# Optimization experiments

Measured on AMD Instinct MI355X. Metric: run time of the kernel, lower is better.

## Reference

```python
import jax, jax.numpy as jnp
import numpy as np

ALPHA = 0.8
TOPK = 9
LOW_BOUND = 0.0
EPS = 1e-10
IOU_EPS = 1e-6


def pairwise_iou(boxes1, boxes2):
    # boxes1 [N,4], boxes2 [G,4] in x1,y1,x2,y2 -> IoU [N,G] (mmdet BboxOverlaps2D)
    area1 = (boxes1[:, 2] - boxes1[:, 0]) * (boxes1[:, 3] - boxes1[:, 1])  # [N]
    area2 = (boxes2[:, 2] - boxes2[:, 0]) * (boxes2[:, 3] - boxes2[:, 1])  # [G]
    lt = jnp.maximum(boxes1[:, None, :2], boxes2[None, :, :2])  # [N,G,2]
    rb = jnp.minimum(boxes1[:, None, 2:], boxes2[None, :, 2:])  # [N,G,2]
    wh = jnp.clip(rb - lt, 0.0)
    inter = wh[..., 0] * wh[..., 1]  # [N,G]
    union = area1[:, None] + area2[None, :] - inter
    return inter / jnp.maximum(union, IOU_EPS)


def setup_inputs() -> dict:
    key = jax.random.key(0)
    k1, k2, k3, k4, k5, k6, k7 = jax.random.split(key, 7)
    N, G, C = 65536, 256, 80
    IMG = 1024.0
    points = jax.random.uniform(k1, (N, 2), dtype=jnp.float32) * IMG  # (cy, cx)
    p_xy1 = jax.random.uniform(k2, (N, 2), dtype=jnp.float32) * (IMG - 96.0)
    p_wh = jax.random.uniform(k3, (N, 2), dtype=jnp.float32) * 95.0 + 1.0
    bbox_preds = jnp.concatenate([p_xy1, p_xy1 + p_wh], axis=1)  # valid x1y1x2y2
    g_xy1 = jax.random.uniform(k4, (G, 2), dtype=jnp.float32) * (IMG - 256.0)
    g_wh = jax.random.uniform(k5, (G, 2), dtype=jnp.float32) * 255.0 + 1.0
    gt_bboxes = jnp.concatenate([g_xy1, g_xy1 + g_wh], axis=1)
    cls_scores = jax.random.normal(k6, (N, C), dtype=jnp.float32)
    gt_labels = jax.random.randint(k7, (G,), 0, C)
    return {"points": points, "cls_scores": cls_scores, "bbox_preds": bbox_preds,
            "gt_bboxes": gt_bboxes, "gt_labels": gt_labels}


def reference(points, cls_scores, bbox_preds, gt_bboxes, gt_labels):
    num_points = points.shape[0]
    num_gt = gt_bboxes.shape[0]
    overlaps = pairwise_iou(bbox_preds, gt_bboxes)  # [N,G]
    cls_cost = jax.nn.sigmoid(cls_scores[:, gt_labels])  # [N,G]
    overlaps = cls_cost ** (1.0 - ALPHA) * overlaps ** ALPHA
    # top-k points per GT (torch: overlaps.topk(k, dim=0))
    _, topk_idxs = jax.lax.top_k(overlaps.T, TOPK)  # [G,K]
    candidate_idxs = topk_idxs.T  # [K,G]
    cp = jnp.transpose(points[candidate_idxs], (1, 0, 2))  # [G,K,2] (cy,cx)
    # mle_2d_gaussian_2: per-GT MLE Gaussian over candidate points
    miu = cp.mean(axis=1, keepdims=True)  # [G,1,2]
    diff = cp - miu  # [G,K,2]
    sigma = jnp.einsum('gki,gkj->gij', diff, diff) / TOPK  # [G,2,2]
    a, b = sigma[:, 0, 0], sigma[:, 0, 1]
    c, d = sigma[:, 1, 0], sigma[:, 1, 1]
    det = a * d - b * c  # [G]
    inv = jnp.stack([jnp.stack([d, -b], axis=-1),
                     jnp.stack([-c, a], axis=-1)], axis=-2) / (det + EPS)[:, None, None]
    maha = jnp.einsum('gki,gij,gkj->gk', diff, inv, diff)  # [G,K]
    candidate_w = jnp.exp(-0.5 * maha).T  # [K,G]
    # center-inside-gt validity, evaluated only at candidate points
    cy, cx = cp[:, :, 0], cp[:, :, 1]  # [G,K]
    gx1, gy1, gx2, gy2 = (gt_bboxes[:, i][:, None] for i in range(4))  # [G,1]
    valid = ((cx - gx1 > EPS) & (cy - gy1 > EPS) &
             (gx2 - cx > EPS) & (gy2 - cy > EPS)).T  # [K,G]
    wv = candidate_w * valid.astype(candidate_w.dtype)
    # scatter per-GT weights to points, then max over GTs == scatter-max
    w = jnp.zeros((num_points,), dtype=cls_scores.dtype)
    w = w.at[candidate_idxs.reshape(-1)].max(wv.reshape(-1))
    w = jnp.where(w < LOW_BOUND, jnp.zeros_like(w), w)
    return w
```

## Files before the change

### kernel.cpp

```cpp
#include <hip/hip_runtime.h>
#include <hip/hip_bf16.h>
#include <math.h>

#define NPTS   65536
#define NGT    256
#define NCLS   80
#define TOPK   9
#define GSLICE 32
#define NPB    256
#define NXB    (NPTS / NPB)
#define SCAP   64

__device__ inline unsigned long long pack_key(float L, unsigned idx) {
    unsigned u   = __float_as_uint(L);
    unsigned k32 = (u & 0x80000000u) ? ~u : (u | 0x80000000u);
    return ((unsigned long long)k32 << 32) | (unsigned)(~idx);
}

__device__ inline unsigned long long umax64(unsigned long long a,
                                            unsigned long long b) {
    return a > b ? a : b;
}

__global__ __launch_bounds__(256) void filter_kernel(
    const float* __restrict__ preds,
    const float* __restrict__ gtb,
    const int*   __restrict__ glab,
    const float* __restrict__ cls,
    unsigned short* __restrict__ counts,
    unsigned long long* __restrict__ bucket,
    float* __restrict__ w)
{
    __shared__ unsigned lcnt[GSLICE];
    __shared__ int      glabs[GSLICE];
    __shared__ unsigned long long stage[GSLICE][SCAP];

    const int t   = threadIdx.x;
    const int xb  = blockIdx.x;
    const int g0  = blockIdx.y * GSLICE;
    const int pt  = xb * NPB + t;
    const int bid = blockIdx.y * NXB + xb;

    if (t < GSLICE) {
        lcnt[t]  = 0u;
        glabs[t] = glab[g0 + t];
    }
    if (t < 32) w[bid * 32 + t] = 0.0f;

    float4 pb = ((const float4*)preds)[pt];
    float parea = (pb.z - pb.x) * (pb.w - pb.y);
    __syncthreads();

    for (int gi = 0; gi < GSLICE; ++gi) {
        const float4 g4 = ((const float4*)gtb)[g0 + gi];
        float ix1 = fmaxf(pb.x, g4.x), iy1 = fmaxf(pb.y, g4.y);
        float ix2 = fminf(pb.z, g4.z), iy2 = fminf(pb.w, g4.w);
        float iw  = fmaxf(ix2 - ix1, 0.0f);
        float ih  = fmaxf(iy2 - iy1, 0.0f);
        float inter = iw * ih;
        if (inter > 0.0f) {
            float garea = (g4.z - g4.x) * (g4.w - g4.y);
            float uni = fmaxf(parea + garea - inter, 1e-6f);
            float iou = inter / uni;
            unsigned long long entry =
                ((unsigned long long)__float_as_uint(iou) << 32) |
                (unsigned)(~(unsigned)pt);
            unsigned slot = atomicAdd(&lcnt[gi], 1u);
            if (slot < SCAP) stage[gi][slot] = entry;
        }
    }
    __syncthreads();

    if (t < GSLICE) {
        unsigned c = lcnt[t];
        if (c > SCAP) c = SCAP;
        lcnt[t] = c;
        counts[(size_t)(g0 + t) * NXB + xb] = (unsigned short)c;
    }
    __syncthreads();

    const float E1 = 1.0f - 0.8f;
#pragma unroll
    for (int k = 0; k < 8; k += 4) {
        unsigned long long e[4];
        bool  vld[4];
        int   gi[4];
        float x[4];
#pragma unroll
        for (int j = 0; j < 4; ++j) {
            int i = (k + j) * 256 + t;
            gi[j] = i >> 6;
            int sl = i & (SCAP - 1);
            e[j]   = stage[gi[j]][sl];
            vld[j] = sl < (int)lcnt[gi[j]];
        }
#pragma unroll
        for (int j = 0; j < 4; ++j) {
            if (vld[j]) {
                unsigned p = ~(unsigned)(e[j] & 0xFFFFFFFFu);
                x[j] = cls[(size_t)p * NCLS + glabs[gi[j]]];
            }
        }
#pragma unroll
        for (int j = 0; j < 4; ++j) {
            if (vld[j]) {
                float iou = __uint_as_float((unsigned)(e[j] >> 32));
                float s   = 1.0f / (1.0f + expf(-x[j]));
                float L   = E1 * log2f(s) + 0.8f * log2f(iou);
                unsigned u   = __float_as_uint(L);
                unsigned k32 = (u & 0x80000000u) ? ~u : (u | 0x80000000u);
                int i = (k + j) * 256 + t;
                bucket[((size_t)(g0 + gi[j]) * NXB + xb) * SCAP + (i & (SCAP - 1))]
                    = ((unsigned long long)k32 << 32) | (e[j] & 0xFFFFFFFFu);
            }
        }
    }
}

__global__ __launch_bounds__(1024) void select_kernel(
    const unsigned short*     __restrict__ counts,
    const unsigned long long* __restrict__ bucket,
    const float* __restrict__ pts,
    const float* __restrict__ gtb,
    float* __restrict__ w)
{
    const int g    = blockIdx.x;
    const int t    = threadIdx.x;
    const int lane = t & 63;
    const int wid  = t >> 6;

    __shared__ unsigned short scnt[NXB];
    __shared__ unsigned long long wmax[16];
    __shared__ unsigned long long winner_s;
    __shared__ unsigned tidx[TOPK];
    __shared__ float ppy[TOPK], ppx[TOPK];

    if (t < NXB) scnt[t] = counts[(size_t)g * NXB + t];
    __syncthreads();

    unsigned long long e[17];
#pragma unroll
    for (int k = 0; k < 16; k += 4) {
#pragma unroll
        for (int j = 0; j < 4; ++j) {
            int i = (k + j) * 1024 + t;
            unsigned long long v = bucket[(size_t)g * (NXB * SCAP) + i];
            bool vld = (i & (SCAP - 1)) < (int)scnt[i >> 6];
            e[k + j] = vld ? v : 0ULL;
        }
    }
    e[16] = (t < TOPK) ? pack_key(-INFINITY, (unsigned)t) : 0ULL;

    unsigned long long mymax = 0ULL;
#pragma unroll
    for (int j = 0; j < 17; ++j) mymax = umax64(mymax, e[j]);

    for (int r = 0; r < TOPK; ++r) {
        unsigned long long m = mymax;
#pragma unroll
        for (int off = 1; off < 64; off <<= 1)
            m = umax64(m, (unsigned long long)__shfl_xor(m, off));
        if (lane == 0) wmax[wid] = m;
        __syncthreads();
        if (t == 0) {
            unsigned long long win = wmax[0];
#pragma unroll
            for (int wv = 1; wv < 16; ++wv) win = umax64(win, wmax[wv]);
            winner_s = win;
            tidx[r]  = ~(unsigned)(win & 0xFFFFFFFFu);
        }
        __syncthreads();
        unsigned long long win = winner_s;
        if (mymax == win) {
#pragma unroll
            for (int j = 0; j < 17; ++j)
                if (e[j] == win) e[j] = 0ULL;
            mymax = 0ULL;
#pragma unroll
            for (int j = 0; j < 17; ++j) mymax = umax64(mymax, e[j]);
        }
    }
    __syncthreads();

    if (t < TOPK) {
        unsigned pi = tidx[t];
        ppy[t] = pts[2 * (size_t)pi];
        ppx[t] = pts[2 * (size_t)pi + 1];
    }
    __syncthreads();

    if (t == 0) {
        float4 g4 = ((const float4*)gtb)[g];
        float m0 = 0.0f, m1 = 0.0f;
#pragma unroll
        for (int k = 0; k < TOPK; ++k) { m0 += ppy[k]; m1 += ppx[k]; }
        m0 /= (float)TOPK; m1 /= (float)TOPK;

        float d0[TOPK], d1[TOPK];
        float a = 0.0f, bb = 0.0f, dd = 0.0f;
#pragma unroll
        for (int k = 0; k < TOPK; ++k) {
            d0[k] = ppy[k] - m0;
            d1[k] = ppx[k] - m1;
            a  += d0[k] * d0[k];
            bb += d0[k] * d1[k];
            dd += d1[k] * d1[k];
        }
        a /= (float)TOPK; bb /= (float)TOPK; dd /= (float)TOPK;
        float det  = a * dd - bb * bb;
        float rinv = 1.0f / (det + 1e-10f);

#pragma unroll
        for (int k = 0; k < TOPK; ++k) {
            float q = d0[k] * (dd * d0[k] - bb * d1[k])
                    + d1[k] * (a  * d1[k] - bb * d0[k]);
            float maha = q * rinv;
            float wt = expf(-0.5f * maha);
            bool valid = (ppx[k] - g4.x > 1e-10f) && (ppy[k] - g4.y > 1e-10f) &&
                         (g4.z - ppx[k] > 1e-10f) && (g4.w - ppy[k] > 1e-10f);
            float wv = valid ? wt : 0.0f;
            atomicMax((int*)&w[tidx[k]], __float_as_int(wv));
        }
    }
}

extern "C" void kernel_launch(void* const* d_in, const int* in_sizes, int n_in,
                              void* d_out, int out_size, void* d_ws, size_t ws_size,
                              hipStream_t stream) {
    const float* points  = (const float*)d_in[0];
    const float* cls     = (const float*)d_in[1];
    const float* preds   = (const float*)d_in[2];
    const float* gtb     = (const float*)d_in[3];
    const int*   glab    = (const int*)d_in[4];
    float* w = (float*)d_out;

    char* ws = (char*)d_ws;
    unsigned long long* bucket = (unsigned long long*)ws;
    size_t off = (size_t)NGT * NXB * SCAP * sizeof(unsigned long long);
    unsigned short* counts = (unsigned short*)(ws + off);

    filter_kernel<<<dim3(NXB, NGT / GSLICE), 256, 0, stream>>>(
        preds, gtb, glab, cls, counts, bucket, w);
    select_kernel<<<NGT, 1024, 0, stream>>>(counts, bucket, points, gtb, w);
}
```

Measured before the change: 113.0 us.

## Cut barriers in top-k selection with double-buffered wave maxima and lazy wave reductions

Each top-k round in select_kernel now uses one barrier instead of two. A double-buffered shared array of per-wave maxima lets every thread compute the block winner redundantly. The 64-lane shuffle reduction is redone only in the wave that held the winner, and bucket loads are skipped for invalid slots. The goal is less barrier and shuffle overhead in the serial 9-round loop, at the cost of each thread reading all 16 wave maxima every round.

```diff
diff --git a/kernel.cpp b/kernel.cpp
--- a/kernel.cpp
+++ b/kernel.cpp
@@ -130,8 +130,7 @@
     const int wid  = t >> 6;
 
     __shared__ unsigned short scnt[NXB];
-    __shared__ unsigned long long wmax[16];
-    __shared__ unsigned long long winner_s;
+    __shared__ unsigned long long wmax[2][16];
     __shared__ unsigned tidx[TOPK];
     __shared__ float ppy[TOPK], ppx[TOPK];
 
@@ -140,14 +139,12 @@
 
     unsigned long long e[17];
 #pragma unroll
-    for (int k = 0; k < 16; k += 4) {
-#pragma unroll
-        for (int j = 0; j < 4; ++j) {
-            int i = (k + j) * 1024 + t;
-            unsigned long long v = bucket[(size_t)g * (NXB * SCAP) + i];
-            bool vld = (i & (SCAP - 1)) < (int)scnt[i >> 6];
-            e[k + j] = vld ? v : 0ULL;
-        }
+    for (int k = 0; k < 16; ++k) {
+        int i = k * 1024 + t;
+        bool vld = lane < (int)scnt[i >> 6];
+        unsigned long long v = 0ULL;
+        if (vld) v = bucket[(size_t)g * (NXB * SCAP) + i];
+        e[k] = v;
     }
     e[16] = (t < TOPK) ? pack_key(-INFINITY, (unsigned)t) : 0ULL;
 
@@ -155,22 +152,20 @@
 #pragma unroll
     for (int j = 0; j < 17; ++j) mymax = umax64(mymax, e[j]);
 
+    unsigned long long wm = mymax;
+#pragma unroll
+    for (int off = 1; off < 64; off <<= 1)
+        wm = umax64(wm, (unsigned long long)__shfl_xor(wm, off));
+
     for (int r = 0; r < TOPK; ++r) {
-        unsigned long long m = mymax;
-#pragma unroll
-        for (int off = 1; off < 64; off <<= 1)
-            m = umax64(m, (unsigned long long)__shfl_xor(m, off));
-        if (lane == 0) wmax[wid] = m;
+        if (lane == 0) wmax[r & 1][wid] = wm;
         __syncthreads();
-        if (t == 0) {
-            unsigned long long win = wmax[0];
-#pragma unroll
-            for (int wv = 1; wv < 16; ++wv) win = umax64(win, wmax[wv]);
-            winner_s = win;
-            tidx[r]  = ~(unsigned)(win & 0xFFFFFFFFu);
-        }
-        __syncthreads();
-        unsigned long long win = winner_s;
+        unsigned long long win = wmax[r & 1][0];
+#pragma unroll
+        for (int wv = 1; wv < 16; ++wv) win = umax64(win, wmax[r & 1][wv]);
+        if (t == 0) tidx[r] = ~(unsigned)(win & 0xFFFFFFFFu);
+
+        bool mine = (wm == win);
         if (mymax == win) {
 #pragma unroll
             for (int j = 0; j < 17; ++j)
@@ -178,6 +173,13 @@
             mymax = 0ULL;
 #pragma unroll
             for (int j = 0; j < 17; ++j) mymax = umax64(mymax, e[j]);
+        }
+        if (mine && r < TOPK - 1) {
+            unsigned long long m = mymax;
+#pragma unroll
+            for (int off = 1; off < 64; off <<= 1)
+                m = umax64(m, (unsigned long long)__shfl_xor(m, off));
+            wm = m;
         }
     }
     __syncthreads();
```

After: 112.6 us. No clear change (-0.3%).
